# Performance work log

Measured on AMD Instinct MI355X. Metric: run time of the kernel, lower is better.

The kernel has to match this reference:

```python
import jax, jax.numpy as jnp
import numpy as np

# Module hyperparameters (from AdaptiveWeightInterpolationModule defaults)
SIGMA_D = 1.5        # gaussian splat bandwidth
TAO_R = 0.05         # truncation threshold on gaussian splat weight
PROW = 2             # splat window: offsets in [-PROW+1, PROW] -> (2*PROW)^2 taps
LAMBDA_E = 30.0 / 255.0
LAMBDA_V = 1.0
NW = 3               # photometric-error averaging window
THRESH = 1e-06
EPS = 1e-06


def _bilinear_warp(img, flow):
    """Backward-warp img [B,C,H,W] by flow [B,2,H,W] (sample at x+u, y+v)."""
    B, C, H, W = img.shape
    xs = jnp.arange(W, dtype=flow.dtype)
    ys = jnp.arange(H, dtype=flow.dtype)
    gx = jnp.clip(xs[None, None, :] + flow[:, 0], 0.0, W - 1.0)  # [B,H,W]
    gy = jnp.clip(ys[None, :, None] + flow[:, 1], 0.0, H - 1.0)
    x0 = jnp.floor(gx); y0 = jnp.floor(gy)
    x1 = jnp.minimum(x0 + 1.0, W - 1.0); y1 = jnp.minimum(y0 + 1.0, H - 1.0)
    wx = (gx - x0)[:, None]; wy = (gy - y0)[:, None]  # [B,1,H,W]
    flat = img.reshape(B, C, H * W)

    def gather(yi, xi):
        idx = (yi * W + xi).astype(jnp.int32).reshape(B, 1, H * W)
        g = jnp.take_along_axis(flat, jnp.broadcast_to(idx, (B, C, H * W)), axis=2)
        return g.reshape(B, C, H, W)

    Ia = gather(y0, x0); Ib = gather(y0, x1)
    Ic = gather(y1, x0); Id = gather(y1, x1)
    return Ia * (1 - wx) * (1 - wy) + Ib * wx * (1 - wy) + Ic * (1 - wx) * wy + Id * wx * wy


def _weight_layer(i1, i2, flow):
    """WeightLayer: photometric-consistency flow weight, [B,1,H,W]."""
    warped = _bilinear_warp(i2, flow)
    err = jnp.mean(jnp.abs(i1 - warped), axis=1, keepdims=True)  # [B,1,H,W]
    k = jnp.ones((1, 1, NW, NW), err.dtype) / float(NW * NW)
    err = jax.lax.conv_general_dilated(err, k, (1, 1), 'SAME',
                                       dimension_numbers=('NCHW', 'OIHW', 'NCHW'))
    return LAMBDA_V * jnp.exp(-(err / LAMBDA_E) ** 2)


def _splat(flow, src):
    """Forward gaussian splat of src [B,C,H,W] along flow [B,2,H,W] -> [B,C,H,W].
    Each source pixel scatters src*exp(-d^2/(2 sigma_d^2)) (truncated at TAO_R)
    to the (2*PROW)^2 integer neighbors of its flow target."""
    B, C, H, W = src.shape
    xs = jnp.arange(W, dtype=flow.dtype)
    ys = jnp.arange(H, dtype=flow.dtype)
    tx = xs[None, None, :] + flow[:, 0]  # [B,H,W]
    ty = ys[None, :, None] + flow[:, 1]
    fx = jnp.floor(tx); fy = jnp.floor(ty)
    boff = (jnp.arange(B) * H * W)[:, None, None]
    srcf = src.transpose(1, 0, 2, 3).reshape(C, B * H * W)
    out = jnp.zeros((C, B * H * W), src.dtype)
    inv2s2 = 1.0 / (2.0 * SIGMA_D * SIGMA_D)
    for dy in range(-PROW + 1, PROW + 1):
        for dx in range(-PROW + 1, PROW + 1):
            ix = fx + dx; iy = fy + dy
            d2 = (tx - ix) ** 2 + (ty - iy) ** 2
            g = jnp.exp(-d2 * inv2s2)
            g = jnp.where(g > TAO_R, g, 0.0)  # tao_r truncation
            valid = (ix >= 0) & (ix < W) & (iy >= 0) & (iy < H)
            g = jnp.where(valid, g, 0.0)
            idx = (boff + jnp.clip(iy, 0, H - 1) * W + jnp.clip(ix, 0, W - 1))
            idx = idx.astype(jnp.int32).reshape(B * H * W)
            out = out.at[:, idx].add(srcf * g.reshape(1, B * H * W))
    return out.reshape(C, B, H, W).transpose(1, 0, 2, 3)


def setup_inputs() -> dict:
    key = jax.random.key(0)
    k1, k2, k3, k4 = jax.random.split(key, 4)
    B, H, W = 4, 720, 1280
    return {
        'input1': jax.random.uniform(k1, (B, 3, H, W), jnp.float32),
        'input2': jax.random.uniform(k2, (B, 3, H, W), jnp.float32),
        'input3': jax.random.normal(k3, (B, 2, H, W), jnp.float32),
        'input4': jax.random.normal(k4, (B, 2, H, W), jnp.float32),
    }


def reference(input1, input2, input3, input4):
    # branch 1: warp frame 1 forward with flow input3
    fw1 = _weight_layer(input1, input2, input3)            # [B,1,H,W]
    p1 = _splat(input3, input1 * fw1)                      # PixelValueLayer
    pw1 = _splat(input3, fw1)                              # PixelWeightLayer
    rw1 = _splat(input3, jnp.ones_like(fw1))               # ReliableWeightLayer
    i1 = p1 / (pw1 + THRESH)
    w1 = pw1 / (rw1 + THRESH)
    # branch 2: warp frame 2 forward with flow input4
    fw2 = _weight_layer(input2, input1, input4)
    p2 = _splat(input4, input2 * fw2)
    pw2 = _splat(input4, fw2)
    rw2 = _splat(input4, jnp.ones_like(fw2))
    i2 = p2 / (pw2 + THRESH)
    w2 = pw2 / (rw2 + THRESH)
    # adaptive blend
    return (i1 * w1 + i2 * w2) / (w1 + w2 + EPS)
```

## Files before the change

kernel.cpp:

```cpp
#include <hip/hip_runtime.h>

#define BATCH 4
#define HGT   720
#define WID   1280
#define HW    (HGT * WID)
#define NPIX  (BATCH * HW)
#define INV2S2 0.22222222222222222f
#define INV_LAMBDA_E (255.0f / 30.0f)
#define THRESH 1e-6f
#define EPSV   1e-6f

#define GT    16
#define GM    5
#define GE    (GT + 2 * GM)
#define GEC   (GE * GE)
#define CUT   4.0f
#define CELLS 19
#define SCOL  20
#define ECAP  208

__global__ __launch_bounds__(256) void err_kernel(
    const float* __restrict__ i1, const float* __restrict__ i2,
    const float* __restrict__ flow, float* __restrict__ err) {
  int n = blockIdx.x * blockDim.x + threadIdx.x;
  if (n >= NPIX) return;
  int b = n / HW;
  int r = n - b * HW;
  int y = r / WID;
  int x = r - y * WID;

  float u = flow[(b * 2 + 0) * HW + r];
  float v = flow[(b * 2 + 1) * HW + r];
  float gx = fminf(fmaxf((float)x + u, 0.0f), (float)(WID - 1));
  float gy = fminf(fmaxf((float)y + v, 0.0f), (float)(HGT - 1));
  float x0f = floorf(gx), y0f = floorf(gy);
  int x0 = (int)x0f, y0 = (int)y0f;
  int x1 = min(x0 + 1, WID - 1), y1 = min(y0 + 1, HGT - 1);
  float wx = gx - x0f, wy = gy - y0f;
  float w00 = (1.0f - wx) * (1.0f - wy);
  float w01 = wx * (1.0f - wy);
  float w10 = (1.0f - wx) * wy;
  float w11 = wx * wy;
  int i00 = y0 * WID + x0, i01 = y0 * WID + x1;
  int i10 = y1 * WID + x0, i11 = y1 * WID + x1;

  const float* i2b = i2 + (size_t)b * 3 * HW;
  const float* i1b = i1 + (size_t)b * 3 * HW;
  float s = 0.0f;
#pragma unroll
  for (int c = 0; c < 3; ++c) {
    const float* p = i2b + c * HW;
    float wv = p[i00] * w00 + p[i01] * w01 + p[i10] * w10 + p[i11] * w11;
    s += fabsf(i1b[c * HW + r] - wv);
  }
  err[n] = s * (1.0f / 3.0f);
}

__global__ __launch_bounds__(256) void fw_kernel(
    const float* __restrict__ err, float* __restrict__ fw) {
  int n = blockIdx.x * blockDim.x + threadIdx.x;
  if (n >= NPIX) return;
  int b = n / HW;
  int r = n - b * HW;
  int y = r / WID;
  int x = r - y * WID;
  const float* e = err + (size_t)b * HW;
  float s = 0.0f;
#pragma unroll
  for (int dy = -1; dy <= 1; ++dy) {
    int yy = y + dy;
    if (yy < 0 || yy >= HGT) continue;
#pragma unroll
    for (int dx = -1; dx <= 1; ++dx) {
      int xx = x + dx;
      if (xx < 0 || xx >= WID) continue;
      s += e[yy * WID + xx];
    }
  }
  s *= (1.0f / 9.0f);
  float t = s * INV_LAMBDA_E;
  fw[n] = expf(-t * t);
}

__global__ __launch_bounds__(256) void splat_binned_kernel(
    const float* __restrict__ flow, const float* __restrict__ img,
    const float* __restrict__ fw, float* __restrict__ p,
    float* __restrict__ pw, float* __restrict__ rw) {
  __shared__ float2 sfrac[GEC];
  __shared__ float4 sval[GEC];
  __shared__ unsigned short sent[CELLS * ECAP];
  __shared__ unsigned int scnt[CELLS * CELLS];
  __shared__ unsigned int sstart[CELLS * SCOL];

  const int b = blockIdx.z;
  const int tx0 = blockIdx.x * GT;
  const int ty0 = blockIdx.y * GT;
  const int ex0 = tx0 - GM;
  const int ey0 = ty0 - GM;
  const float* fu  = flow + (size_t)(b * 2 + 0) * HW;
  const float* fv  = flow + (size_t)(b * 2 + 1) * HW;
  const float* ib  = img + (size_t)b * 3 * HW;
  const float* fwb = fw + (size_t)b * HW;

  for (int i = threadIdx.x; i < CELLS * CELLS; i += 256) scnt[i] = 0u;
  __syncthreads();

  int mycell[3];
  unsigned int myofs[3];
#pragma unroll
  for (int t = 0; t < 3; ++t) {
    int cell = -1;
    unsigned int ofs = 0;
    int i = threadIdx.x + t * 256;
    if (i < GEC) {
      int sly = i / GE, slx = i - sly * GE;
      int sx = ex0 + slx, sy = ey0 + sly;
      if (sx >= 0 && sx < WID && sy >= 0 && sy < HGT) {
        int r = sy * WID + sx;
        float u = fu[r], v = fv[r];
        if (fabsf(u) < CUT && fabsf(v) < CUT) {
          float tx = (float)sx + u;
          float ty = (float)sy + v;
          float fx = floorf(tx), fy = floorf(ty);
          int cx = (int)fx - (tx0 - 2);
          int cy = (int)fy - (ty0 - 2);
          if (cx >= 0 && cx < CELLS && cy >= 0 && cy < CELLS) {
            float fwv = fwb[r];
            sfrac[i] = make_float2(tx - fx, ty - fy);
            sval[i] = make_float4(ib[r] * fwv, ib[HW + r] * fwv,
                                  ib[2 * HW + r] * fwv, fwv);
            cell = cy * CELLS + cx;
            ofs = atomicAdd(&scnt[cell], 1u);
          }
        }
      }
    }
    mycell[t] = cell;
    myofs[t] = ofs;
  }
  __syncthreads();

  for (int c = threadIdx.x; c < CELLS * SCOL; c += 256) {
    int cy = c / SCOL, cx = c - cy * SCOL;
    unsigned int s = 0;
    for (int q = 0; q < cx; ++q) s += scnt[cy * CELLS + q];
    sstart[c] = s;
  }
  __syncthreads();

#pragma unroll
  for (int t = 0; t < 3; ++t) {
    if (mycell[t] >= 0) {
      int cy = mycell[t] / CELLS, cx = mycell[t] - cy * CELLS;
      unsigned int pos = sstart[cy * SCOL + cx] + myofs[t];
      sent[cy * ECAP + pos] =
          (unsigned short)(((unsigned)cx << 10) | (unsigned)(threadIdx.x + t * 256));
    }
  }
  __syncthreads();

  const int lx = threadIdx.x & 15;
  const int ly = threadIdx.x >> 4;
  float a0 = 0.f, a1 = 0.f, a2 = 0.f, apw = 0.f, arw = 0.f;

#pragma unroll
  for (int k = 0; k < 4; ++k) {
    const int cy = ly + k;
    int s = (int)sstart[cy * SCOL + lx];
    int e = (int)sstart[cy * SCOL + lx + 4];
    const float cky = (float)(2 - k);
    const int ebase = cy * ECAP;
    for (int j = s; j < e; ++j) {
      unsigned int en = sent[ebase + j];
      int slot = en & 1023;
      int cx = en >> 10;
      float2 fr = sfrac[slot];
      float ddx = fr.x - (float)(lx - cx + 2);
      float ddy = fr.y - cky;
      float g = __expf(-(ddx * ddx + ddy * ddy) * INV2S2);
      float4 vl = sval[slot];
      a0 += vl.x * g;
      a1 += vl.y * g;
      a2 += vl.z * g;
      apw += vl.w * g;
      arw += g;
    }
  }

  const int gi = b * HW + (ty0 + ly) * WID + tx0 + lx;
  p[gi]            = a0;
  p[NPIX + gi]     = a1;
  p[2 * NPIX + gi] = a2;
  pw[gi]           = apw;
  rw[gi]           = arw;
}

__global__ __launch_bounds__(256) void outlier_kernel(
    const float* __restrict__ flow, const float* __restrict__ img,
    const float* __restrict__ fw, float* __restrict__ p,
    float* __restrict__ pw, float* __restrict__ rw) {
  int n = blockIdx.x * blockDim.x + threadIdx.x;
  if (n >= NPIX) return;
  int b = n / HW;
  int r = n - b * HW;
  float u = flow[(b * 2 + 0) * HW + r];
  float v = flow[(b * 2 + 1) * HW + r];
  if (fabsf(u) < CUT && fabsf(v) < CUT) return;

  int y = r / WID;
  int x = r - y * WID;
  float txf = (float)x + u, tyf = (float)y + v;
  float fx = floorf(txf), fy = floorf(tyf);
  int ixb = (int)fx, iyb = (int)fy;
  float fracx = txf - fx, fracy = tyf - fy;

  float gxv[4], gyv[4];
#pragma unroll
  for (int d = 0; d < 4; ++d) {
    float ddx = fracx - (float)(d - 1);
    gxv[d] = __expf(-ddx * ddx * INV2S2);
    float ddy = fracy - (float)(d - 1);
    gyv[d] = __expf(-ddy * ddy * INV2S2);
  }

  float fwv = fw[n];
  const float* ib = img + (size_t)b * 3 * HW;
  float s0 = ib[0 * HW + r] * fwv;
  float s1 = ib[1 * HW + r] * fwv;
  float s2 = ib[2 * HW + r] * fwv;

  int base = b * HW;
  for (int dy = 0; dy < 4; ++dy) {
    int iy = iyb + dy - 1;
    if (iy < 0 || iy >= HGT) continue;
    float gy = gyv[dy];
    for (int dx = 0; dx < 4; ++dx) {
      int ix = ixb + dx - 1;
      if (ix < 0 || ix >= WID) continue;
      float g = gxv[dx] * gy;
      int gi = base + iy * WID + ix;
      atomicAdd(p + gi, s0 * g);
      atomicAdd(p + NPIX + gi, s1 * g);
      atomicAdd(p + 2 * NPIX + gi, s2 * g);
      atomicAdd(pw + gi, fwv * g);
      atomicAdd(rw + gi, g);
    }
  }
}

__global__ __launch_bounds__(256) void acc1_kernel(
    const float* __restrict__ p, const float* __restrict__ pw,
    const float* __restrict__ rw, float* __restrict__ out,
    float* __restrict__ den) {
  int n = blockIdx.x * blockDim.x + threadIdx.x;
  if (n >= NPIX) return;
  int b = n / HW;
  int r = n - b * HW;
  float pwv = pw[n], rwv = rw[n];
  float w = pwv / (rwv + THRESH);
  den[n] = w;
  float scale = w / (pwv + THRESH);
  int ob = b * 3 * HW + r;
  out[ob + 0 * HW] = p[n] * scale;
  out[ob + 1 * HW] = p[NPIX + n] * scale;
  out[ob + 2 * HW] = p[2 * NPIX + n] * scale;
}

__global__ __launch_bounds__(256) void acc2_kernel(
    const float* __restrict__ p, const float* __restrict__ pw,
    const float* __restrict__ rw, const float* __restrict__ den,
    float* __restrict__ out) {
  int n = blockIdx.x * blockDim.x + threadIdx.x;
  if (n >= NPIX) return;
  int b = n / HW;
  int r = n - b * HW;
  float pwv = pw[n], rwv = rw[n];
  float w = pwv / (rwv + THRESH);
  float scale = w / (pwv + THRESH);
  float d = den[n] + w + EPSV;
  float invd = 1.0f / d;
  int ob = b * 3 * HW + r;
  out[ob + 0 * HW] = (out[ob + 0 * HW] + p[n] * scale) * invd;
  out[ob + 1 * HW] = (out[ob + 1 * HW] + p[NPIX + n] * scale) * invd;
  out[ob + 2 * HW] = (out[ob + 2 * HW] + p[2 * NPIX + n] * scale) * invd;
}

extern "C" void kernel_launch(void* const* d_in, const int* in_sizes, int n_in,
                              void* d_out, int out_size, void* d_ws,
                              size_t ws_size, hipStream_t stream) {
  const float* input1 = (const float*)d_in[0];
  const float* input2 = (const float*)d_in[1];
  const float* flow3  = (const float*)d_in[2];
  const float* flow4  = (const float*)d_in[3];
  float* out = (float*)d_out;

  float* ws  = (float*)d_ws;
  float* p   = ws;
  float* err = ws;
  float* pw  = ws + (size_t)3 * NPIX;
  float* rw  = ws + (size_t)4 * NPIX;
  float* fw  = ws + (size_t)5 * NPIX;
  float* den = ws + (size_t)6 * NPIX;

  const int threads = 256;
  const int blocks = (NPIX + threads - 1) / threads;
  dim3 sgrid(WID / GT, HGT / GT, BATCH);

  err_kernel<<<blocks, threads, 0, stream>>>(input1, input2, flow3, err);
  fw_kernel<<<blocks, threads, 0, stream>>>(err, fw);
  splat_binned_kernel<<<sgrid, threads, 0, stream>>>(flow3, input1, fw, p, pw, rw);
  outlier_kernel<<<blocks, threads, 0, stream>>>(flow3, input1, fw, p, pw, rw);
  acc1_kernel<<<blocks, threads, 0, stream>>>(p, pw, rw, out, den);

  err_kernel<<<blocks, threads, 0, stream>>>(input2, input1, flow4, err);
  fw_kernel<<<blocks, threads, 0, stream>>>(err, fw);
  splat_binned_kernel<<<sgrid, threads, 0, stream>>>(flow4, input2, fw, p, pw, rw);
  outlier_kernel<<<blocks, threads, 0, stream>>>(flow4, input2, fw, p, pw, rw);
  acc2_kernel<<<blocks, threads, 0, stream>>>(p, pw, rw, den, out);
}
```

Before: 574.1 us.

## Vectorize elementwise kernels to float4 and fuse both accumulations into one blend

The err, fw and outlier kernels now each process four adjacent pixels per thread, using float4 loads and stores for flow, err and fw. The 3x3 box filter shares loaded row values across the four outputs. When the workspace is large enough, both branches keep separate p/pw/rw buffers, and a single vectorized blend kernel replaces acc1 and acc2, which removes the den buffer round trip and the read-modify-write of out. The cost is a larger workspace, and the outlier kernel now skips only when all four pixels are inliers, which can add per-thread divergence.

```diff
diff --git a/kernel.cpp b/kernel.cpp
--- a/kernel.cpp
+++ b/kernel.cpp
@@ -5,6 +5,7 @@
 #define WID   1280
 #define HW    (HGT * WID)
 #define NPIX  (BATCH * HW)
+#define NQUAD (NPIX / 4)
 #define INV2S2 0.22222222222222222f
 #define INV_LAMBDA_E (255.0f / 30.0f)
 #define THRESH 1e-6f
@@ -22,64 +23,83 @@
 __global__ __launch_bounds__(256) void err_kernel(
     const float* __restrict__ i1, const float* __restrict__ i2,
     const float* __restrict__ flow, float* __restrict__ err) {
-  int n = blockIdx.x * blockDim.x + threadIdx.x;
-  if (n >= NPIX) return;
-  int b = n / HW;
-  int r = n - b * HW;
-  int y = r / WID;
-  int x = r - y * WID;
-
-  float u = flow[(b * 2 + 0) * HW + r];
-  float v = flow[(b * 2 + 1) * HW + r];
-  float gx = fminf(fmaxf((float)x + u, 0.0f), (float)(WID - 1));
-  float gy = fminf(fmaxf((float)y + v, 0.0f), (float)(HGT - 1));
-  float x0f = floorf(gx), y0f = floorf(gy);
-  int x0 = (int)x0f, y0 = (int)y0f;
-  int x1 = min(x0 + 1, WID - 1), y1 = min(y0 + 1, HGT - 1);
-  float wx = gx - x0f, wy = gy - y0f;
-  float w00 = (1.0f - wx) * (1.0f - wy);
-  float w01 = wx * (1.0f - wy);
-  float w10 = (1.0f - wx) * wy;
-  float w11 = wx * wy;
-  int i00 = y0 * WID + x0, i01 = y0 * WID + x1;
-  int i10 = y1 * WID + x0, i11 = y1 * WID + x1;
-
+  int q = blockIdx.x * blockDim.x + threadIdx.x;
+  if (q >= NQUAD) return;
+  int n0 = q * 4;
+  int b = n0 / HW;
+  int r0 = n0 - b * HW;
+  int y = r0 / WID;
+  int x0 = r0 - y * WID;
+
+  const float4 uq = *(const float4*)(flow + (size_t)(b * 2 + 0) * HW + r0);
+  const float4 vq = *(const float4*)(flow + (size_t)(b * 2 + 1) * HW + r0);
+  const float* up = &uq.x;
+  const float* vp = &vq.x;
   const float* i2b = i2 + (size_t)b * 3 * HW;
   const float* i1b = i1 + (size_t)b * 3 * HW;
-  float s = 0.0f;
-#pragma unroll
-  for (int c = 0; c < 3; ++c) {
-    const float* p = i2b + c * HW;
-    float wv = p[i00] * w00 + p[i01] * w01 + p[i10] * w10 + p[i11] * w11;
-    s += fabsf(i1b[c * HW + r] - wv);
-  }
-  err[n] = s * (1.0f / 3.0f);
+
+  float4 eo;
+  float* ep = &eo.x;
+#pragma unroll
+  for (int i = 0; i < 4; ++i) {
+    int x = x0 + i;
+    int r = r0 + i;
+    float gx = fminf(fmaxf((float)x + up[i], 0.0f), (float)(WID - 1));
+    float gy = fminf(fmaxf((float)y + vp[i], 0.0f), (float)(HGT - 1));
+    float x0f = floorf(gx), y0f = floorf(gy);
+    int xa = (int)x0f, ya = (int)y0f;
+    int xb = min(xa + 1, WID - 1), yb = min(ya + 1, HGT - 1);
+    float wx = gx - x0f, wy = gy - y0f;
+    float w00 = (1.0f - wx) * (1.0f - wy);
+    float w01 = wx * (1.0f - wy);
+    float w10 = (1.0f - wx) * wy;
+    float w11 = wx * wy;
+    int i00 = ya * WID + xa, i01 = ya * WID + xb;
+    int i10 = yb * WID + xa, i11 = yb * WID + xb;
+    float s = 0.0f;
+#pragma unroll
+    for (int c = 0; c < 3; ++c) {
+      const float* pl = i2b + c * HW;
+      float wv = pl[i00] * w00 + pl[i01] * w01 + pl[i10] * w10 + pl[i11] * w11;
+      s += fabsf(i1b[c * HW + r] - wv);
+    }
+    ep[i] = s * (1.0f / 3.0f);
+  }
+  *(float4*)(err + n0) = eo;
 }
 
 __global__ __launch_bounds__(256) void fw_kernel(
     const float* __restrict__ err, float* __restrict__ fw) {
-  int n = blockIdx.x * blockDim.x + threadIdx.x;
-  if (n >= NPIX) return;
-  int b = n / HW;
-  int r = n - b * HW;
-  int y = r / WID;
-  int x = r - y * WID;
+  int q = blockIdx.x * blockDim.x + threadIdx.x;
+  if (q >= NQUAD) return;
+  int n0 = q * 4;
+  int b = n0 / HW;
+  int r0 = n0 - b * HW;
+  int y = r0 / WID;
+  int x0 = r0 - y * WID;
   const float* e = err + (size_t)b * HW;
-  float s = 0.0f;
+
+  float s0 = 0.f, s1 = 0.f, s2 = 0.f, s3 = 0.f;
 #pragma unroll
   for (int dy = -1; dy <= 1; ++dy) {
     int yy = y + dy;
     if (yy < 0 || yy >= HGT) continue;
-#pragma unroll
-    for (int dx = -1; dx <= 1; ++dx) {
-      int xx = x + dx;
-      if (xx < 0 || xx >= WID) continue;
-      s += e[yy * WID + xx];
-    }
-  }
-  s *= (1.0f / 9.0f);
-  float t = s * INV_LAMBDA_E;
-  fw[n] = expf(-t * t);
+    const float* row = e + yy * WID;
+    float4 qv = *(const float4*)(row + x0);
+    float l = (x0 > 0) ? row[x0 - 1] : 0.0f;
+    float r = (x0 + 4 < WID) ? row[x0 + 4] : 0.0f;
+    s0 += l + qv.x + qv.y;
+    s1 += qv.x + qv.y + qv.z;
+    s2 += qv.y + qv.z + qv.w;
+    s3 += qv.z + qv.w + r;
+  }
+  float4 o;
+  float t;
+  t = s0 * (1.0f / 9.0f) * INV_LAMBDA_E; o.x = expf(-t * t);
+  t = s1 * (1.0f / 9.0f) * INV_LAMBDA_E; o.y = expf(-t * t);
+  t = s2 * (1.0f / 9.0f) * INV_LAMBDA_E; o.z = expf(-t * t);
+  t = s3 * (1.0f / 9.0f) * INV_LAMBDA_E; o.w = expf(-t * t);
+  *(float4*)(fw + n0) = o;
 }
 
 __global__ __launch_bounds__(256) void splat_binned_kernel(
@@ -199,52 +219,110 @@
     const float* __restrict__ flow, const float* __restrict__ img,
     const float* __restrict__ fw, float* __restrict__ p,
     float* __restrict__ pw, float* __restrict__ rw) {
-  int n = blockIdx.x * blockDim.x + threadIdx.x;
-  if (n >= NPIX) return;
-  int b = n / HW;
-  int r = n - b * HW;
-  float u = flow[(b * 2 + 0) * HW + r];
-  float v = flow[(b * 2 + 1) * HW + r];
-  if (fabsf(u) < CUT && fabsf(v) < CUT) return;
-
-  int y = r / WID;
-  int x = r - y * WID;
-  float txf = (float)x + u, tyf = (float)y + v;
-  float fx = floorf(txf), fy = floorf(tyf);
-  int ixb = (int)fx, iyb = (int)fy;
-  float fracx = txf - fx, fracy = tyf - fy;
-
-  float gxv[4], gyv[4];
-#pragma unroll
-  for (int d = 0; d < 4; ++d) {
-    float ddx = fracx - (float)(d - 1);
-    gxv[d] = __expf(-ddx * ddx * INV2S2);
-    float ddy = fracy - (float)(d - 1);
-    gyv[d] = __expf(-ddy * ddy * INV2S2);
-  }
-
-  float fwv = fw[n];
+  int q = blockIdx.x * blockDim.x + threadIdx.x;
+  if (q >= NQUAD) return;
+  int n0 = q * 4;
+  int b = n0 / HW;
+  int r0 = n0 - b * HW;
+  const float4 uq = *(const float4*)(flow + (size_t)(b * 2 + 0) * HW + r0);
+  const float4 vq = *(const float4*)(flow + (size_t)(b * 2 + 1) * HW + r0);
+  const float* up = &uq.x;
+  const float* vp = &vq.x;
+
+  bool any = false;
+#pragma unroll
+  for (int i = 0; i < 4; ++i)
+    any |= !(fabsf(up[i]) < CUT && fabsf(vp[i]) < CUT);
+  if (!any) return;
+
   const float* ib = img + (size_t)b * 3 * HW;
-  float s0 = ib[0 * HW + r] * fwv;
-  float s1 = ib[1 * HW + r] * fwv;
-  float s2 = ib[2 * HW + r] * fwv;
-
   int base = b * HW;
-  for (int dy = 0; dy < 4; ++dy) {
-    int iy = iyb + dy - 1;
-    if (iy < 0 || iy >= HGT) continue;
-    float gy = gyv[dy];
-    for (int dx = 0; dx < 4; ++dx) {
-      int ix = ixb + dx - 1;
-      if (ix < 0 || ix >= WID) continue;
-      float g = gxv[dx] * gy;
-      int gi = base + iy * WID + ix;
-      atomicAdd(p + gi, s0 * g);
-      atomicAdd(p + NPIX + gi, s1 * g);
-      atomicAdd(p + 2 * NPIX + gi, s2 * g);
-      atomicAdd(pw + gi, fwv * g);
-      atomicAdd(rw + gi, g);
-    }
+#pragma unroll
+  for (int i = 0; i < 4; ++i) {
+    float u = up[i], v = vp[i];
+    if (fabsf(u) < CUT && fabsf(v) < CUT) continue;
+    int r = r0 + i;
+    int y = r / WID;
+    int x = r - y * WID;
+    float txf = (float)x + u, tyf = (float)y + v;
+    float fx = floorf(txf), fy = floorf(tyf);
+    int ixb = (int)fx, iyb = (int)fy;
+    float fracx = txf - fx, fracy = tyf - fy;
+
+    float gxv[4], gyv[4];
+#pragma unroll
+    for (int d = 0; d < 4; ++d) {
+      float ddx = fracx - (float)(d - 1);
+      gxv[d] = __expf(-ddx * ddx * INV2S2);
+      float ddy = fracy - (float)(d - 1);
+      gyv[d] = __expf(-ddy * ddy * INV2S2);
+    }
+
+    float fwv = fw[b * HW + r];
+    float s0 = ib[0 * HW + r] * fwv;
+    float s1 = ib[1 * HW + r] * fwv;
+    float s2 = ib[2 * HW + r] * fwv;
+
+    for (int dy = 0; dy < 4; ++dy) {
+      int iy = iyb + dy - 1;
+      if (iy < 0 || iy >= HGT) continue;
+      float gy = gyv[dy];
+      for (int dx = 0; dx < 4; ++dx) {
+        int ix = ixb + dx - 1;
+        if (ix < 0 || ix >= WID) continue;
+        float g = gxv[dx] * gy;
+        int gi = base + iy * WID + ix;
+        atomicAdd(p + gi, s0 * g);
+        atomicAdd(p + NPIX + gi, s1 * g);
+        atomicAdd(p + 2 * NPIX + gi, s2 * g);
+        atomicAdd(pw + gi, fwv * g);
+        atomicAdd(rw + gi, g);
+      }
+    }
+  }
+}
+
+__global__ __launch_bounds__(256) void blend_kernel(
+    const float* __restrict__ p1, const float* __restrict__ pw1,
+    const float* __restrict__ rw1, const float* __restrict__ p2,
+    const float* __restrict__ pw2, const float* __restrict__ rw2,
+    float* __restrict__ out) {
+  int q = blockIdx.x * blockDim.x + threadIdx.x;
+  if (q >= NQUAD) return;
+  int n0 = q * 4;
+  int b = n0 / HW;
+  int r0 = n0 - b * HW;
+
+  float4 pw1v = *(const float4*)(pw1 + n0);
+  float4 rw1v = *(const float4*)(rw1 + n0);
+  float4 pw2v = *(const float4*)(pw2 + n0);
+  float4 rw2v = *(const float4*)(rw2 + n0);
+  const float* pw1p = &pw1v.x; const float* rw1p = &rw1v.x;
+  const float* pw2p = &pw2v.x; const float* rw2p = &rw2v.x;
+
+  float s1v[4], s2v[4], iv[4];
+#pragma unroll
+  for (int i = 0; i < 4; ++i) {
+    float w1 = pw1p[i] / (rw1p[i] + THRESH);
+    float s1 = w1 / (pw1p[i] + THRESH);
+    float w2 = pw2p[i] / (rw2p[i] + THRESH);
+    float s2 = w2 / (pw2p[i] + THRESH);
+    s1v[i] = s1; s2v[i] = s2;
+    iv[i] = 1.0f / (w1 + w2 + EPSV);
+  }
+
+  size_t ob = (size_t)b * 3 * HW + r0;
+#pragma unroll
+  for (int c = 0; c < 3; ++c) {
+    float4 a = *(const float4*)(p1 + (size_t)c * NPIX + n0);
+    float4 bq = *(const float4*)(p2 + (size_t)c * NPIX + n0);
+    const float* ap = &a.x; const float* bp = &bq.x;
+    float4 o;
+    float* op = &o.x;
+#pragma unroll
+    for (int i = 0; i < 4; ++i)
+      op[i] = (ap[i] * s1v[i] + bp[i] * s2v[i]) * iv[i];
+    *(float4*)(out + ob + (size_t)c * HW) = o;
   }
 }
 
@@ -293,28 +371,50 @@
   const float* flow3  = (const float*)d_in[2];
   const float* flow4  = (const float*)d_in[3];
   float* out = (float*)d_out;
-
   float* ws  = (float*)d_ws;
-  float* p   = ws;
-  float* err = ws;
-  float* pw  = ws + (size_t)3 * NPIX;
-  float* rw  = ws + (size_t)4 * NPIX;
-  float* fw  = ws + (size_t)5 * NPIX;
-  float* den = ws + (size_t)6 * NPIX;
 
   const int threads = 256;
-  const int blocks = (NPIX + threads - 1) / threads;
+  const int qblocks = (NQUAD + threads - 1) / threads;
+  const int nblocks = (NPIX + threads - 1) / threads;
   dim3 sgrid(WID / GT, HGT / GT, BATCH);
 
-  err_kernel<<<blocks, threads, 0, stream>>>(input1, input2, flow3, err);
-  fw_kernel<<<blocks, threads, 0, stream>>>(err, fw);
-  splat_binned_kernel<<<sgrid, threads, 0, stream>>>(flow3, input1, fw, p, pw, rw);
-  outlier_kernel<<<blocks, threads, 0, stream>>>(flow3, input1, fw, p, pw, rw);
-  acc1_kernel<<<blocks, threads, 0, stream>>>(p, pw, rw, out, den);
-
-  err_kernel<<<blocks, threads, 0, stream>>>(input2, input1, flow4, err);
-  fw_kernel<<<blocks, threads, 0, stream>>>(err, fw);
-  splat_binned_kernel<<<sgrid, threads, 0, stream>>>(flow4, input2, fw, p, pw, rw);
-  outlier_kernel<<<blocks, threads, 0, stream>>>(flow4, input2, fw, p, pw, rw);
-  acc2_kernel<<<blocks, threads, 0, stream>>>(p, pw, rw, den, out);
-}
+  if (ws_size >= (size_t)11 * NPIX * sizeof(float)) {
+    float* p1  = ws;
+    float* pw1 = ws + (size_t)3 * NPIX;
+    float* rw1 = ws + (size_t)4 * NPIX;
+    float* p2  = ws + (size_t)5 * NPIX;
+    float* pw2 = ws + (size_t)8 * NPIX;
+    float* rw2 = ws + (size_t)9 * NPIX;
+    float* fw  = ws + (size_t)10 * NPIX;
+    float* err = p2;
+
+    err_kernel<<<qblocks, threads, 0, stream>>>(input1, input2, flow3, err);
+    fw_kernel<<<qblocks, threads, 0, stream>>>(err, fw);
+    splat_binned_kernel<<<sgrid, threads, 0, stream>>>(flow3, input1, fw, p1, pw1, rw1);
+    outlier_kernel<<<qblocks, threads, 0, stream>>>(flow3, input1, fw, p1, pw1, rw1);
+    err_kernel<<<qblocks, threads, 0, stream>>>(input2, input1, flow4, err);
+    fw_kernel<<<qblocks, threads, 0, stream>>>(err, fw);
+    splat_binned_kernel<<<sgrid, threads, 0, stream>>>(flow4, input2, fw, p2, pw2, rw2);
+    outlier_kernel<<<qblocks, threads, 0, stream>>>(flow4, input2, fw, p2, pw2, rw2);
+    blend_kernel<<<qblocks, threads, 0, stream>>>(p1, pw1, rw1, p2, pw2, rw2, out);
+  } else {
+    float* p   = ws;
+    float* err = ws;
+    float* pw  = ws + (size_t)3 * NPIX;
+    float* rw  = ws + (size_t)4 * NPIX;
+    float* fw  = ws + (size_t)5 * NPIX;
+    float* den = ws + (size_t)6 * NPIX;
+
+    err_kernel<<<qblocks, threads, 0, stream>>>(input1, input2, flow3, err);
+    fw_kernel<<<qblocks, threads, 0, stream>>>(err, fw);
+    splat_binned_kernel<<<sgrid, threads, 0, stream>>>(flow3, input1, fw, p, pw, rw);
+    outlier_kernel<<<qblocks, threads, 0, stream>>>(flow3, input1, fw, p, pw, rw);
+    acc1_kernel<<<nblocks, threads, 0, stream>>>(p, pw, rw, out, den);
+
+    err_kernel<<<qblocks, threads, 0, stream>>>(input2, input1, flow4, err);
+    fw_kernel<<<qblocks, threads, 0, stream>>>(err, fw);
+    splat_binned_kernel<<<sgrid, threads, 0, stream>>>(flow4, input2, fw, p, pw, rw);
+    outlier_kernel<<<qblocks, threads, 0, stream>>>(flow4, input2, fw, p, pw, rw);
+    acc2_kernel<<<nblocks, threads, 0, stream>>>(p, pw, rw, den, out);
+  }
+}
```

Result: faster. 558.3 us (-2.8%).
